# Optimization experiments

Measured on AMD Instinct MI355X. Metric: run time of the kernel, lower is better.

## Reference

```python
import jax, jax.numpy as jnp
import numpy as np

N_NODES = 50000
N_EDGES = 625000
D = 128          # hidden_dim
H = 8            # num_heads
DH = D // H      # head_dim
L = 4            # num_layers
F_IN = 64        # in_channels
G = 64           # num graphs
BETA = 1.0
EPS = 1e-5       # layernorm eps


def _seg_softmax(s, idx, n):
    # softmax of s over segments defined by idx (segments present in idx are never empty)
    m = jax.ops.segment_max(s, idx, num_segments=n)
    e = jnp.exp(s - m[idx])
    d = jax.ops.segment_sum(e, idx, num_segments=n)
    return e / d[idx]


def _ln(x, s, b):
    mu = jnp.mean(x, axis=-1, keepdims=True)
    var = jnp.var(x, axis=-1, keepdims=True)
    return (x - mu) / jnp.sqrt(var + EPS) * s + b


def _forward(x, edge_index, batch, node_W, node_b, cW1, cb1, cW2, cb2,
             qW, qb, kW, kb, vW, vb, oW, ob, bW, bb,
             f1W, f1b, f2W, f2b, n1s, n1b, n2s, n2b,
             outW1, outb1, outW2, outb2):
    N = x.shape[0]
    src, tgt = edge_index[0], edge_index[1]
    h = x @ node_W + node_b                              # [N, D]
    for l in range(L):
        # ---- dynamic curvature (attention-approximated Wasserstein) ----
        h_src, h_tgt = h[src], h[tgt]                    # [E, D]
        sim = jnp.sum(h_src * h_tgt, axis=-1) * BETA     # [E]
        alpha = _seg_softmax(sim, tgt, N)                # segment softmax over tgt
        dist = jnp.linalg.norm(h_src - h_tgt, axis=-1)   # [E]
        agg = jax.ops.segment_sum(alpha * dist, tgt, num_segments=N)
        curv = 1.0 - agg[tgt] / jnp.maximum(dist, 1e-6)  # [E]
        ce = jax.nn.relu(curv[:, None] @ cW1 + cb1) @ cW2 + cb2  # [E, D]
        # ---- CurvphormerLayer ----
        xn = _ln(h, n1s[l], n1b[l])
        q = (xn @ qW[l] + qb[l]).reshape(N, H, DH)
        k = (xn @ kW[l] + kb[l]).reshape(N, H, DH)
        v = (xn @ vW[l] + vb[l]).reshape(N, H, DH)
        scores = jnp.sum(q[src] * k[tgt], axis=-1) / (DH ** 0.5)  # [E, H]
        scores = scores + ce @ bW[l] + bb[l]                       # curvature bias
        probs = _seg_softmax(scores, tgt, N)                       # [E, H]
        msgs = (probs[..., None] * v[tgt]).reshape(-1, D)          # [E, D]
        aggm = jax.ops.segment_sum(msgs, src, num_segments=N)     # scatter to src
        h = h + (aggm @ oW[l] + ob[l])
        xn2 = _ln(h, n2s[l], n2b[l])
        h = h + (jax.nn.relu(xn2 @ f1W[l] + f1b[l]) @ f2W[l] + f2b[l])
    # ---- mean pool per graph ----
    counts = jnp.maximum(jax.ops.segment_sum(jnp.ones((N,), h.dtype), batch, num_segments=G), 1.0)
    g = jax.ops.segment_sum(h, batch, num_segments=G) / counts[:, None]
    return jax.nn.relu(g @ outW1 + outb1) @ outW2 + outb2


def setup_inputs() -> dict:
    keys = iter(jax.random.split(jax.random.key(0), 32))
    p = lambda shape, s=0.02: jax.random.normal(next(keys), shape, jnp.float32) * s
    x = jax.random.normal(next(keys), (N_NODES, F_IN), jnp.float32)
    edge_index = jax.random.randint(next(keys), (2, N_EDGES), 0, N_NODES)
    batch = jnp.sort(jax.random.randint(next(keys), (N_NODES,), 0, G))
    inp = {
        "x": x, "edge_index": edge_index, "batch": batch,
        "node_W": p((F_IN, D)), "node_b": p((D,)),
        "cW1": p((1, D)), "cb1": p((D,)), "cW2": p((D, D)), "cb2": p((D,)),
        "qW": p((L, D, D)), "qb": p((L, D)),
        "kW": p((L, D, D)), "kb": p((L, D)),
        "vW": p((L, D, D)), "vb": p((L, D)),
        "oW": p((L, D, D)), "ob": p((L, D)),
        "bW": p((L, D, H)), "bb": p((L, H)),
        "f1W": p((L, D, 4 * D)), "f1b": p((L, 4 * D)),
        "f2W": p((L, 4 * D, D)), "f2b": p((L, D)),
        "n1s": jnp.ones((L, D), jnp.float32), "n1b": jnp.zeros((L, D), jnp.float32),
        "n2s": jnp.ones((L, D), jnp.float32), "n2b": jnp.zeros((L, D), jnp.float32),
        "outW1": p((D, D // 2)), "outb1": p((D // 2,)),
        "outW2": p((D // 2, 1)), "outb2": p((1,)),
    }
    return inp


def reference(x, edge_index, batch, node_W, node_b, cW1, cb1, cW2, cb2,
              qW, qb, kW, kb, vW, vb, oW, ob, bW, bb,
              f1W, f1b, f2W, f2b, n1s, n1b, n2s, n2b,
              outW1, outb1, outW2, outb2):
    return _forward(x, edge_index, batch, node_W, node_b, cW1, cb1, cW2, cb2,
                    qW, qb, kW, kb, vW, vb, oW, ob, bW, bb,
                    f1W, f1b, f2W, f2b, n1s, n1b, n2s, n2b,
                    outW1, outb1, outW2, outb2)
```

## Files before the change

kernel.cpp:

```cpp
#include <hip/hip_runtime.h>

#define NN 50000
#define NE 625000
#define DD 128
#define HH 8
#define DHH 16
#define NL 4
#define FIN 64
#define NG 64
#define LN_EPS 1e-5f
#define NSEG 129
#define NT32 1563
#define NT64 782
#define NBS 196
#define HLP 132

typedef __bf16 bf16x8_t __attribute__((ext_vector_type(8)));
typedef unsigned short ushort8_t __attribute__((ext_vector_type(8)));
typedef float f32x4_t __attribute__((ext_vector_type(4)));
union BF8 { ushort8_t u; bf16x8_t b; };

__device__ __forceinline__ void fma4(float4& a, float s, float4 w) {
  a.x = fmaf(s, w.x, a.x); a.y = fmaf(s, w.y, a.y);
  a.z = fmaf(s, w.z, a.z); a.w = fmaf(s, w.w, a.w);
}
__device__ __forceinline__ unsigned short f2bf(float f) {
  unsigned u = __float_as_uint(f);
  unsigned r = ((u >> 16) & 1u) + 0x7FFFu;
  return (unsigned short)((u + r) >> 16);
}
__device__ __forceinline__ float bf2f(unsigned short u) {
  return __uint_as_float((unsigned)u << 16);
}

__device__ __forceinline__ void ln_tile_bf32(const float* __restrict__ h, int nb,
                                             const float* __restrict__ sc,
                                             const float* __restrict__ bi,
                                             ushort* xbf) {
  int tid = threadIdx.x;
  int r = tid >> 4, l16 = tid & 15;
  int nr = nb + r; if (nr >= NN) nr = NN - 1;
  const float* hp = h + (size_t)nr * DD + l16 * 8;
  float4 a0 = *(const float4*)hp;
  float4 a1 = *(const float4*)(hp + 4);
  float sum = a0.x + a0.y + a0.z + a0.w + a1.x + a1.y + a1.z + a1.w;
  float sq  = a0.x*a0.x + a0.y*a0.y + a0.z*a0.z + a0.w*a0.w
            + a1.x*a1.x + a1.y*a1.y + a1.z*a1.z + a1.w*a1.w;
#pragma unroll
  for (int off = 8; off >= 1; off >>= 1) {
    sum += __shfl_xor(sum, off, 64);
    sq  += __shfl_xor(sq,  off, 64);
  }
  float mu   = sum * (1.0f / DD);
  float var  = sq * (1.0f / DD) - mu * mu;
  float rstd = rsqrtf(var + LN_EPS);
  int d0 = l16 * 8;
  float4 s0 = *(const float4*)(sc + d0), s1 = *(const float4*)(sc + d0 + 4);
  float4 b0 = *(const float4*)(bi + d0), b1 = *(const float4*)(bi + d0 + 4);
  ushort8_t u;
  u[0] = f2bf((a0.x - mu) * rstd * s0.x + b0.x);
  u[1] = f2bf((a0.y - mu) * rstd * s0.y + b0.y);
  u[2] = f2bf((a0.z - mu) * rstd * s0.z + b0.z);
  u[3] = f2bf((a0.w - mu) * rstd * s0.w + b0.w);
  u[4] = f2bf((a1.x - mu) * rstd * s1.x + b1.x);
  u[5] = f2bf((a1.y - mu) * rstd * s1.y + b1.y);
  u[6] = f2bf((a1.z - mu) * rstd * s1.z + b1.z);
  u[7] = f2bf((a1.w - mu) * rstd * s1.w + b1.w);
  int off = (r * 256 + l16 * 16) ^ ((r & 7) << 4);
  *(ushort8_t*)((char*)xbf + off) = u;
}

__global__ __launch_bounds__(256) void k_node_proj(const float* __restrict__ x,
                                                   const float* __restrict__ W,
                                                   const float* __restrict__ b,
                                                   float* __restrict__ h) {
  __shared__ float Wl[FIN * DD];
  __shared__ float xt[32][FIN];
  int tid = threadIdx.x;
  int nb = blockIdx.x * 32;
  for (int i = tid * 4; i < FIN * DD; i += 1024)
    *(float4*)&Wl[i] = *(const float4*)(W + i);
  for (int i = tid * 4; i < 32 * FIN; i += 1024) {
    int row = i >> 6, cc = i & 63;
    int node = nb + row; if (node >= NN) node = NN - 1;
    *(float4*)&xt[row][cc] = *(const float4*)(x + (size_t)node * FIN + cc);
  }
  __syncthreads();
  int c4 = (tid & 31) * 4;
  int r0 = (tid >> 5) * 4;
  float4 bv = *(const float4*)(b + c4);
  float4 a0 = bv, a1 = bv, a2 = bv, a3 = bv;
  for (int k = 0; k < FIN; k++) {
    float4 wv = *(const float4*)&Wl[k * DD + c4];
    fma4(a0, xt[r0][k], wv);
    fma4(a1, xt[r0 + 1][k], wv);
    fma4(a2, xt[r0 + 2][k], wv);
    fma4(a3, xt[r0 + 3][k], wv);
  }
  int n0 = nb + r0;
  if (n0 < NN)     *(float4*)(h + (size_t)n0 * DD + c4) = a0;
  if (n0 + 1 < NN) *(float4*)(h + (size_t)(n0 + 1) * DD + c4) = a1;
  if (n0 + 2 < NN) *(float4*)(h + (size_t)(n0 + 2) * DD + c4) = a2;
  if (n0 + 3 < NN) *(float4*)(h + (size_t)(n0 + 3) * DD + c4) = a3;
}

__global__ __launch_bounds__(256) void k_edge1(const int* __restrict__ src_s, const int* __restrict__ tgt_s,
                                               const float* __restrict__ h, float* __restrict__ sim,
                                               float* __restrict__ dist) {
  int gid = blockIdx.x * 256 + threadIdx.x;
  int e = gid >> 4;
  if (e >= NE) return;
  int j = gid & 15;
  int s = src_s[e], t = tgt_s[e];
  const float4* ap = (const float4*)(h + (size_t)s * DD + j * 8);
  const float4* bp = (const float4*)(h + (size_t)t * DD + j * 8);
  float4 a0 = ap[0], a1 = ap[1];
  float4 b0 = bp[0], b1 = bp[1];
  float dot = 0.f, sq = 0.f;
  dot = fmaf(a0.x, b0.x, dot); dot = fmaf(a0.y, b0.y, dot);
  dot = fmaf(a0.z, b0.z, dot); dot = fmaf(a0.w, b0.w, dot);
  dot = fmaf(a1.x, b1.x, dot); dot = fmaf(a1.y, b1.y, dot);
  dot = fmaf(a1.z, b1.z, dot); dot = fmaf(a1.w, b1.w, dot);
  float d0 = a0.x - b0.x, d1 = a0.y - b0.y, d2 = a0.z - b0.z, d3 = a0.w - b0.w;
  float d4 = a1.x - b1.x, d5 = a1.y - b1.y, d6 = a1.z - b1.z, d7 = a1.w - b1.w;
  sq = fmaf(d0, d0, sq); sq = fmaf(d1, d1, sq); sq = fmaf(d2, d2, sq); sq = fmaf(d3, d3, sq);
  sq = fmaf(d4, d4, sq); sq = fmaf(d5, d5, sq); sq = fmaf(d6, d6, sq); sq = fmaf(d7, d7, sq);
#pragma unroll
  for (int off = 8; off >= 1; off >>= 1) {
    dot += __shfl_xor(dot, off, 64);
    sq  += __shfl_xor(sq,  off, 64);
  }
  if (j == 0) {
    sim[e]  = dot;
    dist[e] = sqrtf(sq);
  }
}

__global__ __launch_bounds__(256) void k_curva(const int* __restrict__ rowstart_t,
    const int* __restrict__ eid_t, const float* __restrict__ sim,
    const float* __restrict__ dist, float* __restrict__ aggv) {
  int node = blockIdx.x * 32 + (threadIdx.x >> 3);
  if (node >= NN) return;
  int j = threadIdx.x & 7;
  int rs = rowstart_t[node], re = rowstart_t[node + 1];
  float m = -3.4e38f;
  for (int i = rs + j; i < re; i += 8) m = fmaxf(m, sim[eid_t[i]]);
#pragma unroll
  for (int off = 1; off <= 4; off <<= 1) m = fmaxf(m, __shfl_xor(m, off, 64));
  float den = 0.f, nd = 0.f;
  for (int i = rs + j; i < re; i += 8) {
    int e = eid_t[i];
    float ev = expf(sim[e] - m);
    den += ev;
    nd = fmaf(ev, dist[e], nd);
  }
#pragma unroll
  for (int off = 1; off <= 4; off <<= 1) {
    den += __shfl_xor(den, off, 64);
    nd  += __shfl_xor(nd,  off, 64);
  }
  if (j == 0) aggv[node] = den > 0.f ? nd / den : 0.f;
}

__global__ __launch_bounds__(512) void k_ln_qkv(const float* __restrict__ h,
    const float* __restrict__ n1s_l, const float* __restrict__ n1b_l,
    const ushort* __restrict__ qkvT_l,
    const float* __restrict__ qb_l, const float* __restrict__ kb_l, const float* __restrict__ vb_l,
    ushort* __restrict__ q, ushort* __restrict__ kk, ushort* __restrict__ v) {
  __shared__ __align__(16) ushort xbf[32 * DD];
  int nb = blockIdx.x * 32;
  ln_tile_bf32(h, nb, n1s_l, n1b_l, xbf);
  __syncthreads();
  int lane = threadIdx.x & 63;
  int w = threadIdx.x >> 6;
  int g = lane >> 4, c = lane & 15;
  int xr = (c & 7) << 4;
  char* xb = (char*)xbf;
  BF8 a[2][4];
#pragma unroll
  for (int nt = 0; nt < 2; nt++)
#pragma unroll
    for (int kt = 0; kt < 4; kt++)
      a[nt][kt].u = *(ushort8_t*)(xb + (((nt * 16 + c) * 256 + kt * 64 + g * 16) ^ xr));
#pragma unroll
  for (int ti = 0; ti < 3; ti++) {
    int t = w * 3 + ti;
    int m = t >> 3;
    int colb = (t & 7) * 16;
    const float* bias = (m == 0 ? qb_l : (m == 1 ? kb_l : vb_l));
    float4 bv = *(const float4*)(bias + colb + g * 4);
    f32x4_t acc0 = {bv.x, bv.y, bv.z, bv.w};
    f32x4_t acc1 = acc0;
    const ushort* wp = qkvT_l + (size_t)(m * DD + colb + c) * DD + g * 8;
#pragma unroll
    for (int kt = 0; kt < 4; kt++) {
      BF8 b; b.u = *(const ushort8_t*)(wp + kt * 32);
      acc0 = __builtin_amdgcn_mfma_f32_16x16x32_bf16(b.b, a[0][kt].b, acc0, 0, 0, 0);
      acc1 = __builtin_amdgcn_mfma_f32_16x16x32_bf16(b.b, a[1][kt].b, acc1, 0, 0, 0);
    }
    ushort* out = (m == 0 ? q : (m == 1 ? kk : v));
    int n0 = nb + c;
    if (n0 < NN) {
      ushort4 o; o.x = f2bf(acc0[0]); o.y = f2bf(acc0[1]); o.z = f2bf(acc0[2]); o.w = f2bf(acc0[3]);
      *(ushort4*)(out + (size_t)n0 * DD + colb + g * 4) = o;
    }
    int n1 = nb + 16 + c;
    if (n1 < NN) {
      ushort4 o; o.x = f2bf(acc1[0]); o.y = f2bf(acc1[1]); o.z = f2bf(acc1[2]); o.w = f2bf(acc1[3]);
      *(ushort4*)(out + (size_t)n1 * DD + colb + g * 4) = o;
    }
  }
}

__global__ __launch_bounds__(256) void k_scores(const int* __restrict__ src_s, const int* __restrict__ tgt_s,
    const ushort* __restrict__ q, const ushort* __restrict__ k,
    const float* __restrict__ dist, const float* __restrict__ aggv,
    const float* __restrict__ bp_g,
    const float* __restrict__ slope_l, const float* __restrict__ inter_l,
    float* __restrict__ escore) {
  __shared__ float lsl[NSEG * HH], lin[NSEG * HH], bp[DD];
  __shared__ float lcurv[32];
  __shared__ int   lseg[32];
  int tid = threadIdx.x;
  for (int idx = tid; idx < NSEG * HH; idx += 256) { lsl[idx] = slope_l[idx]; lin[idx] = inter_l[idx]; }
  if (tid < DD) bp[tid] = bp_g[tid];
  __syncthreads();
  int eb = blockIdx.x * 32;
  if (tid < 32) {
    int e = eb + tid;
    if (e < NE) {
      int t = tgt_s[e];
      float curv = 1.0f - aggv[t] / fmaxf(dist[e], 1e-6f);
      int lo = 0, hi = DD;
      while (lo < hi) { int mid = (lo + hi) >> 1; if (bp[mid] < curv) lo = mid + 1; else hi = mid; }
      lcurv[tid] = curv;
      lseg[tid] = lo;
    }
  }
  __syncthreads();
  int gi = blockIdx.x * 256 + tid;
  if (gi >= NE * HH) return;
  int i = gi >> 3, hh = gi & 7;
  int s = src_s[i], t = tgt_s[i];
  int li = tid >> 3;
  float curv = lcurv[li];
  int seg = lseg[li];
  float bias = fmaf(lsl[seg * HH + hh], curv, lin[seg * HH + hh]);
  const ushort8_t* qp = (const ushort8_t*)(q + (size_t)s * DD + hh * DHH);
  const ushort8_t* kp = (const ushort8_t*)(k + (size_t)t * DD + hh * DHH);
  float dot = 0.f;
#pragma unroll
  for (int ii = 0; ii < 2; ii++) {
    ushort8_t a = qp[ii], b = kp[ii];
#pragma unroll
    for (int jj = 0; jj < 8; jj++) dot = fmaf(bf2f(a[jj]), bf2f(b[jj]), dot);
  }
  escore[gi] = dot * 0.25f + bias;
  (void)t;
}

__global__ __launch_bounds__(256) void k_softmax_t(const int* __restrict__ rowstart_t,
    const int* __restrict__ eid_t, const float* __restrict__ escore, float2* __restrict__ msd) {
  int node = blockIdx.x * 32 + (threadIdx.x >> 3);
  if (node >= NN) return;
  int hh = threadIdx.x & 7;
  int rs = rowstart_t[node], re = rowstart_t[node + 1];
  float m = -3.4e38f;
  int i = rs;
  for (; i + 4 <= re; i += 4) {
    int e0 = eid_t[i], e1 = eid_t[i + 1], e2 = eid_t[i + 2], e3 = eid_t[i + 3];
    float s0 = escore[e0 * HH + hh];
    float s1 = escore[e1 * HH + hh];
    float s2 = escore[e2 * HH + hh];
    float s3 = escore[e3 * HH + hh];
    m = fmaxf(m, s0); m = fmaxf(m, s1); m = fmaxf(m, s2); m = fmaxf(m, s3);
  }
  for (; i < re; i++) m = fmaxf(m, escore[eid_t[i] * HH + hh]);
  float sum = 0.f;
  i = rs;
  for (; i + 4 <= re; i += 4) {
    int e0 = eid_t[i], e1 = eid_t[i + 1], e2 = eid_t[i + 2], e3 = eid_t[i + 3];
    float p0 = expf(escore[e0 * HH + hh] - m);
    float p1 = expf(escore[e1 * HH + hh] - m);
    float p2 = expf(escore[e2 * HH + hh] - m);
    float p3 = expf(escore[e3 * HH + hh] - m);
    sum += p0; sum += p1; sum += p2; sum += p3;
  }
  for (; i < re; i++) sum += expf(escore[eid_t[i] * HH + hh] - m);
  float2 o; o.x = m; o.y = sum > 0.f ? 1.0f / sum : 0.f;
  msd[(size_t)node * HH + hh] = o;
}

__global__ __launch_bounds__(256) void k_agg(const int* __restrict__ tgt_s,
    const int* __restrict__ rowstart,
    const float* __restrict__ escore, const float2* __restrict__ msd,
    const ushort* __restrict__ v, ushort* __restrict__ aggmb) {
  int wave = (blockIdx.x * 256 + threadIdx.x) >> 6;
  int lane = threadIdx.x & 63;
  int rs = rowstart[wave], re = rowstart[wave + 1];
  int hh = lane >> 3;
  int d = lane * 2;
  float a0 = 0.f, a1 = 0.f;
  int i = rs;
  for (; i + 4 <= re; i += 4) {
    int t0 = tgt_s[i], t1 = tgt_s[i + 1], t2 = tgt_s[i + 2], t3 = tgt_s[i + 3];
    float e0 = escore[(i    ) * HH + hh];
    float e1 = escore[(i + 1) * HH + hh];
    float e2 = escore[(i + 2) * HH + hh];
    float e3 = escore[(i + 3) * HH + hh];
    float2 m0 = msd[(size_t)t0 * HH + hh], m1 = msd[(size_t)t1 * HH + hh];
    float2 m2 = msd[(size_t)t2 * HH + hh], m3 = msd[(size_t)t3 * HH + hh];
    ushort2 v0 = *(const ushort2*)(v + (size_t)t0 * DD + d);
    ushort2 v1 = *(const ushort2*)(v + (size_t)t1 * DD + d);
    ushort2 v2 = *(const ushort2*)(v + (size_t)t2 * DD + d);
    ushort2 v3 = *(const ushort2*)(v + (size_t)t3 * DD + d);
    float p0 = expf(e0 - m0.x) * m0.y;
    float p1 = expf(e1 - m1.x) * m1.y;
    float p2 = expf(e2 - m2.x) * m2.y;
    float p3 = expf(e3 - m3.x) * m3.y;
    a0 = fmaf(p0, bf2f(v0.x), a0); a1 = fmaf(p0, bf2f(v0.y), a1);
    a0 = fmaf(p1, bf2f(v1.x), a0); a1 = fmaf(p1, bf2f(v1.y), a1);
    a0 = fmaf(p2, bf2f(v2.x), a0); a1 = fmaf(p2, bf2f(v2.y), a1);
    a0 = fmaf(p3, bf2f(v3.x), a0); a1 = fmaf(p3, bf2f(v3.y), a1);
  }
  for (; i < re; i++) {
    int t = tgt_s[i];
    float2 md = msd[(size_t)t * HH + hh];
    float prob = expf(escore[i * HH + hh] - md.x) * md.y;
    ushort2 vv = *(const ushort2*)(v + (size_t)t * DD + d);
    a0 = fmaf(prob, bf2f(vv.x), a0);
    a1 = fmaf(prob, bf2f(vv.y), a1);
  }
  ushort2 o; o.x = f2bf(a0); o.y = f2bf(a1);
  *(ushort2*)(aggmb + (size_t)wave * DD + d) = o;
}

__global__ __launch_bounds__(512) void k_attn_ffn(const ushort* __restrict__ aggmb,
    const ushort* __restrict__ oT_l, const float* __restrict__ ob_l,
    const float* __restrict__ n2s_l, const float* __restrict__ n2b_l,
    const ushort* __restrict__ f1T_l, const float* __restrict__ f1b_l,
    const ushort* __restrict__ f2T_l, const float* __restrict__ f2b_l,
    float* __restrict__ h) {
  __shared__ float hL[64 * HLP];
  __shared__ __align__(16) char ubuf[64 * 256 * 2];
  ushort* xbf = (ushort*)ubuf;
  char* xb = ubuf;
  char* tb = ubuf;
  int nb = blockIdx.x * 64;
  int tid = threadIdx.x;
  int lane = tid & 63, w = tid >> 6;
  int g = lane >> 4, c = lane & 15;
  int colb = w * 16;
  int xr = (c & 7) << 4;
  {
    float4 obv = *(const float4*)(ob_l + colb + g * 4);
    const ushort* wp = oT_l + (size_t)(colb + c) * DD + g * 8;
    BF8 b0, b1, b2, b3;
    b0.u = *(const ushort8_t*)(wp);
    b1.u = *(const ushort8_t*)(wp + 32);
    b2.u = *(const ushort8_t*)(wp + 64);
    b3.u = *(const ushort8_t*)(wp + 96);
#pragma unroll
    for (int nt = 0; nt < 4; nt++) {
      int node = nb + nt * 16 + c;
      int na = node < NN ? node : NN - 1;
      const ushort* ap = aggmb + (size_t)na * DD + g * 8;
      BF8 a0, a1, a2, a3;
      a0.u = *(const ushort8_t*)(ap);
      a1.u = *(const ushort8_t*)(ap + 32);
      a2.u = *(const ushort8_t*)(ap + 64);
      a3.u = *(const ushort8_t*)(ap + 96);
      f32x4_t acc = {obv.x, obv.y, obv.z, obv.w};
      acc = __builtin_amdgcn_mfma_f32_16x16x32_bf16(b0.b, a0.b, acc, 0, 0, 0);
      acc = __builtin_amdgcn_mfma_f32_16x16x32_bf16(b1.b, a1.b, acc, 0, 0, 0);
      acc = __builtin_amdgcn_mfma_f32_16x16x32_bf16(b2.b, a2.b, acc, 0, 0, 0);
      acc = __builtin_amdgcn_mfma_f32_16x16x32_bf16(b3.b, a3.b, acc, 0, 0, 0);
      float4 hv = *(const float4*)(h + (size_t)na * DD + colb + g * 4);
      hv.x += acc[0]; hv.y += acc[1]; hv.z += acc[2]; hv.w += acc[3];
      *(float4*)&hL[(nt * 16 + c) * HLP + colb + g * 4] = hv;
    }
  }
  __syncthreads();
  {
    int l16 = tid & 15;
    int d0 = l16 * 8;
    float4 s0 = *(const float4*)(n2s_l + d0), s1 = *(const float4*)(n2s_l + d0 + 4);
    float4 bb0 = *(const float4*)(n2b_l + d0), bb1 = *(const float4*)(n2b_l + d0 + 4);
#pragma unroll
    for (int p = 0; p < 2; p++) {
      int r = p * 32 + (tid >> 4);
      const float* hp = &hL[r * HLP + d0];
      float4 a0 = *(const float4*)hp;
      float4 a1 = *(const float4*)(hp + 4);
      float sum = a0.x + a0.y + a0.z + a0.w + a1.x + a1.y + a1.z + a1.w;
      float sq  = a0.x*a0.x + a0.y*a0.y + a0.z*a0.z + a0.w*a0.w
                + a1.x*a1.x + a1.y*a1.y + a1.z*a1.z + a1.w*a1.w;
#pragma unroll
      for (int off = 8; off >= 1; off >>= 1) {
        sum += __shfl_xor(sum, off, 64);
        sq  += __shfl_xor(sq,  off, 64);
      }
      float mu   = sum * (1.0f / DD);
      float var  = sq * (1.0f / DD) - mu * mu;
      float rstd = rsqrtf(var + LN_EPS);
      ushort8_t u;
      u[0] = f2bf((a0.x - mu) * rstd * s0.x + bb0.x);
      u[1] = f2bf((a0.y - mu) * rstd * s0.y + bb0.y);
      u[2] = f2bf((a0.z - mu) * rstd * s0.z + bb0.z);
      u[3] = f2bf((a0.w - mu) * rstd * s0.w + bb0.w);
      u[4] = f2bf((a1.x - mu) * rstd * s1.x + bb1.x);
      u[5] = f2bf((a1.y - mu) * rstd * s1.y + bb1.y);
      u[6] = f2bf((a1.z - mu) * rstd * s1.z + bb1.z);
      u[7] = f2bf((a1.w - mu) * rstd * s1.w + bb1.w);
      int off = (r * 256 + l16 * 16) ^ ((r & 7) << 4);
      *(ushort8_t*)(xb + off) = u;
    }
  }
  __syncthreads();
  BF8 a[4][4];
#pragma unroll
  for (int nt = 0; nt < 4; nt++)
#pragma unroll
    for (int kt = 0; kt < 4; kt++)
      a[nt][kt].u = *(ushort8_t*)(xb + (((nt * 16 + c) * 256 + kt * 64 + g * 16) ^ xr));
  __syncthreads();
  float4 bv2 = *(const float4*)(f2b_l + colb + g * 4);
  f32x4_t o0 = {bv2.x, bv2.y, bv2.z, bv2.w};
  f32x4_t o1 = o0, o2 = o0, o3 = o0;
#pragma unroll
  for (int ch = 0; ch < 2; ch++) {
    if (ch) __syncthreads();
#pragma unroll
    for (int ti = 0; ti < 2; ti++) {
      int ctile = w * 2 + ti;
      int col = ch * 256 + ctile * 16;
      float4 bv = *(const float4*)(f1b_l + col + g * 4);
      f32x4_t ac0 = {bv.x, bv.y, bv.z, bv.w};
      f32x4_t ac1 = ac0, ac2 = ac0, ac3 = ac0;
      const ushort* wp = f1T_l + (size_t)(col + c) * DD + g * 8;
#pragma unroll
      for (int kt = 0; kt < 4; kt++) {
        BF8 b; b.u = *(const ushort8_t*)(wp + kt * 32);
        ac0 = __builtin_amdgcn_mfma_f32_16x16x32_bf16(b.b, a[0][kt].b, ac0, 0, 0, 0);
        ac1 = __builtin_amdgcn_mfma_f32_16x16x32_bf16(b.b, a[1][kt].b, ac1, 0, 0, 0);
        ac2 = __builtin_amdgcn_mfma_f32_16x16x32_bf16(b.b, a[2][kt].b, ac2, 0, 0, 0);
        ac3 = __builtin_amdgcn_mfma_f32_16x16x32_bf16(b.b, a[3][kt].b, ac3, 0, 0, 0);
      }
      int colL = (ctile * 16 + g * 4) * 2;
      {
        int row = c;
        ushort4 o4; o4.x = f2bf(fmaxf(ac0[0], 0.f)); o4.y = f2bf(fmaxf(ac0[1], 0.f));
        o4.z = f2bf(fmaxf(ac0[2], 0.f)); o4.w = f2bf(fmaxf(ac0[3], 0.f));
        *(ushort4*)(tb + ((row * 512 + colL) ^ ((row & 7) << 4))) = o4;
      }
      {
        int row = 16 + c;
        ushort4 o4; o4.x = f2bf(fmaxf(ac1[0], 0.f)); o4.y = f2bf(fmaxf(ac1[1], 0.f));
        o4.z = f2bf(fmaxf(ac1[2], 0.f)); o4.w = f2bf(fmaxf(ac1[3], 0.f));
        *(ushort4*)(tb + ((row * 512 + colL) ^ ((row & 7) << 4))) = o4;
      }
      {
        int row = 32 + c;
        ushort4 o4; o4.x = f2bf(fmaxf(ac2[0], 0.f)); o4.y = f2bf(fmaxf(ac2[1], 0.f));
        o4.z = f2bf(fmaxf(ac2[2], 0.f)); o4.w = f2bf(fmaxf(ac2[3], 0.f));
        *(ushort4*)(tb + ((row * 512 + colL) ^ ((row & 7) << 4))) = o4;
      }
      {
        int row = 48 + c;
        ushort4 o4; o4.x = f2bf(fmaxf(ac3[0], 0.f)); o4.y = f2bf(fmaxf(ac3[1], 0.f));
        o4.z = f2bf(fmaxf(ac3[2], 0.f)); o4.w = f2bf(fmaxf(ac3[3], 0.f));
        *(ushort4*)(tb + ((row * 512 + colL) ^ ((row & 7) << 4))) = o4;
      }
    }
    __syncthreads();
    const ushort* wp2 = f2T_l + (size_t)(colb + c) * 512 + ch * 256 + g * 8;
#pragma unroll
    for (int kt = 0; kt < 8; kt++) {
      BF8 b; b.u = *(const ushort8_t*)(wp2 + kt * 32);
      BF8 t0; t0.u = *(ushort8_t*)(tb + (((c) * 512 + kt * 64 + g * 16) ^ xr));
      BF8 t1; t1.u = *(ushort8_t*)(tb + (((16 + c) * 512 + kt * 64 + g * 16) ^ xr));
      BF8 t2; t2.u = *(ushort8_t*)(tb + (((32 + c) * 512 + kt * 64 + g * 16) ^ xr));
      BF8 t3; t3.u = *(ushort8_t*)(tb + (((48 + c) * 512 + kt * 64 + g * 16) ^ xr));
      o0 = __builtin_amdgcn_mfma_f32_16x16x32_bf16(b.b, t0.b, o0, 0, 0, 0);
      o1 = __builtin_amdgcn_mfma_f32_16x16x32_bf16(b.b, t1.b, o1, 0, 0, 0);
      o2 = __builtin_amdgcn_mfma_f32_16x16x32_bf16(b.b, t2.b, o2, 0, 0, 0);
      o3 = __builtin_amdgcn_mfma_f32_16x16x32_bf16(b.b, t3.b, o3, 0, 0, 0);
    }
  }
  {
    int node = nb + c;
    if (node < NN) {
      const float* lp = &hL[c * HLP + colb + g * 4];
      float4 hv = *(const float4*)lp;
      hv.x += o0[0]; hv.y += o0[1]; hv.z += o0[2]; hv.w += o0[3];
      *(float4*)(h + (size_t)node * DD + colb + g * 4) = hv;
    }
  }
  {
    int node = nb + 16 + c;
    if (node < NN) {
      const float* lp = &hL[(16 + c) * HLP + colb + g * 4];
      float4 hv = *(const float4*)lp;
      hv.x += o1[0]; hv.y += o1[1]; hv.z += o1[2]; hv.w += o1[3];
      *(float4*)(h + (size_t)node * DD + colb + g * 4) = hv;
    }
  }
  {
    int node = nb + 32 + c;
    if (node < NN) {
      const float* lp = &hL[(32 + c) * HLP + colb + g * 4];
      float4 hv = *(const float4*)lp;
      hv.x += o2[0]; hv.y += o2[1]; hv.z += o2[2]; hv.w += o2[3];
      *(float4*)(h + (size_t)node * DD + colb + g * 4) = hv;
    }
  }
  {
    int node = nb + 48 + c;
    if (node < NN) {
      const float* lp = &hL[(48 + c) * HLP + colb + g * 4];
      float4 hv = *(const float4*)lp;
      hv.x += o3[0]; hv.y += o3[1]; hv.z += o3[2]; hv.w += o3[3];
      *(float4*)(h + (size_t)node * DD + colb + g * 4) = hv;
    }
  }
}

template <int K, int C>
__global__ void k_wt(const float* __restrict__ W, ushort* __restrict__ WT, int nm, int dstride) {
  int idx = blockIdx.x * 256 + threadIdx.x;
  if (idx >= K * C * nm) return;
  int mi = idx / (K * C), rem = idx - mi * (K * C);
  int cc = rem / K, kk2 = rem - cc * K;
  WT[(size_t)mi * dstride + cc * K + kk2] = f2bf(W[(size_t)mi * K * C + (size_t)kk2 * C + cc]);
}

__global__ void k_hist(const int* __restrict__ idxs, int* __restrict__ cnt) {
  int e = blockIdx.x * 256 + threadIdx.x;
  if (e < NE) atomicAdd(cnt + idxs[e], 1);
}

__global__ __launch_bounds__(256) void k_scan_blk(const int* __restrict__ cnt, int* __restrict__ bsum) {
  __shared__ int red[256];
  int tid = threadIdx.x;
  int idx = blockIdx.x * 256 + tid;
  red[tid] = (idx < NN) ? cnt[idx] : 0;
  __syncthreads();
  for (int off = 128; off >= 1; off >>= 1) {
    if (tid < off) red[tid] += red[tid + off];
    __syncthreads();
  }
  if (tid == 0) bsum[blockIdx.x] = red[0];
}

__global__ __launch_bounds__(256) void k_scan_top(const int* __restrict__ bsum,
                                                  int* __restrict__ boff, int* __restrict__ rowstart) {
  __shared__ int ps[256];
  int t = threadIdx.x;
  int v = (t < NBS) ? bsum[t] : 0;
  ps[t] = v;
  __syncthreads();
  for (int off = 1; off < 256; off <<= 1) {
    int x = (t >= off) ? ps[t - off] : 0;
    __syncthreads();
    ps[t] += x;
    __syncthreads();
  }
  boff[t] = ps[t] - v;
  if (t == 255) rowstart[NN] = ps[255];
}

__global__ __launch_bounds__(256) void k_scan_fin(const int* __restrict__ cnt,
                                                  const int* __restrict__ boff, int* __restrict__ rowstart) {
  __shared__ int ps[256];
  int t = threadIdx.x;
  int idx = blockIdx.x * 256 + t;
  int v = (idx < NN) ? cnt[idx] : 0;
  ps[t] = v;
  __syncthreads();
  for (int off = 1; off < 256; off <<= 1) {
    int x = (t >= off) ? ps[t - off] : 0;
    __syncthreads();
    ps[t] += x;
    __syncthreads();
  }
  if (idx < NN) rowstart[idx] = boff[blockIdx.x] + ps[t] - v;
}

__global__ void k_fill(const int* __restrict__ src, const int* __restrict__ tgt,
                       const int* __restrict__ rowstart,
                       int* __restrict__ cur, int* __restrict__ src_s, int* __restrict__ tgt_s) {
  int e = blockIdx.x * 256 + threadIdx.x;
  if (e >= NE) return;
  int s = src[e];
  int p = atomicAdd(cur + s, 1);
  int pos = rowstart[s] + p;
  src_s[pos] = s;
  tgt_s[pos] = tgt[e];
}

__global__ void k_fill_t(const int* __restrict__ tgt_s, const int* __restrict__ rowstart_t,
                         int* __restrict__ cur_t, int* __restrict__ eid_t) {
  int i = blockIdx.x * 256 + threadIdx.x;
  if (i >= NE) return;
  int t = tgt_s[i];
  int p = atomicAdd(cur_t + t, 1);
  eid_t[rowstart_t[t] + p] = i;
}

__global__ __launch_bounds__(64) void k_mbias_par(const float* __restrict__ cW2, const float* __restrict__ cb2,
                                                  const float* __restrict__ bW, const float* __restrict__ bb,
                                                  float* __restrict__ M, float* __restrict__ base) {
  int bid = blockIdx.x;
  int l = bid >> 7, d = bid & 127;
  int lane = threadIdx.x;
  int hh = lane >> 3, j0 = lane & 7;
  const float* bWl = bW + (size_t)l * DD * HH;
  float acc = 0.f;
#pragma unroll
  for (int t = 0; t < 16; t++) {
    int k = j0 + t * 8;
    acc = fmaf(cW2[d * DD + k], bWl[k * HH + hh], acc);
  }
#pragma unroll
  for (int off = 1; off <= 4; off <<= 1) acc += __shfl_xor(acc, off, 64);
  if (j0 == 0) M[(size_t)l * DD * HH + d * HH + hh] = acc;
  if (d == 0) {
    float bacc = 0.f;
#pragma unroll
    for (int t = 0; t < 16; t++) {
      int k = j0 + t * 8;
      bacc = fmaf(cb2[k], bWl[k * HH + hh], bacc);
    }
#pragma unroll
    for (int off = 1; off <= 4; off <<= 1) bacc += __shfl_xor(bacc, off, 64);
    if (j0 == 0) base[l * HH + hh] = bacc + bb[l * HH + hh];
  }
}

__global__ __launch_bounds__(128) void k_bp(const float* __restrict__ cW1, const float* __restrict__ cb1,
                                            float* __restrict__ bpg, int* __restrict__ posg) {
  __shared__ float x[DD], bp[DD];
  int tid = threadIdx.x;
  float c1v = cW1[tid], cbv = cb1[tid];
  x[tid] = (c1v == 0.f) ? __builtin_inff() : (-cbv / c1v);
  __syncthreads();
  float xv = x[tid]; int p = 0;
  for (int j = 0; j < DD; j++) {
    float xj = x[j];
    if (xj < xv || (xj == xv && j < tid)) p++;
  }
  bp[p] = xv;
  posg[tid] = p;
  __syncthreads();
  bpg[tid] = bp[tid];
}

__global__ __launch_bounds__(64) void k_pwl_tab(const float* __restrict__ cW1, const float* __restrict__ cb1,
    const int* __restrict__ posg, const float* __restrict__ Mb, const float* __restrict__ basel,
    float* __restrict__ slopeg, float* __restrict__ interg) {
  int bid = blockIdx.x;
  int l = bid / NSEG, s = bid - l * NSEG;
  int lane = threadIdx.x;
  int hh = lane >> 3, j0 = lane & 7;
  const float* M = Mb + (size_t)l * DD * HH;
  float sl = 0.f, in = 0.f;
#pragma unroll
  for (int t = 0; t < 16; t++) {
    int d = j0 + t * 8;
    float cv = cW1[d], cbv = cb1[d];
    int p = posg[d];
    bool act = (cv == 0.f) ? (cbv > 0.f) : ((cv > 0.f) ? (p < s) : (p >= s));
    float m = act ? M[d * HH + hh] : 0.f;
    sl = fmaf(cv, m, sl);
    in = fmaf(cbv, m, in);
  }
#pragma unroll
  for (int off = 1; off <= 4; off <<= 1) {
    sl += __shfl_xor(sl, off, 64);
    in += __shfl_xor(in, off, 64);
  }
  if (j0 == 0) {
    size_t o = (size_t)l * NSEG * HH + s * HH + hh;
    slopeg[o] = sl;
    interg[o] = in + basel[l * HH + hh];
  }
}

__global__ void k_bounds(const int* __restrict__ batch, int* __restrict__ gstart, int* __restrict__ gend) {
  int n = blockIdx.x * 256 + threadIdx.x;
  if (n >= NN) return;
  int b = batch[n];
  if (n == 0 || batch[n - 1] != b) gstart[b] = n;
  if (n == NN - 1 || batch[n + 1] != b) gend[b] = n + 1;
}

__global__ __launch_bounds__(256) void k_pool_part(const float* __restrict__ h,
    const int* __restrict__ batch, float* __restrict__ gpool) {
  int tid = threadIdx.x;
  int d = tid & 127, sub = tid >> 7;
  int n0 = blockIdx.x * 256;
  int nend = n0 + 256; if (nend > NN) nend = NN;
  float run = 0.f; int gcur = -1;
  for (int n = n0 + sub; n < nend; n += 2) {
    int g = batch[n];
    if (g != gcur) {
      if (gcur >= 0) atomicAdd(gpool + (size_t)gcur * DD + d, run);
      run = 0.f; gcur = g;
    }
    run += h[(size_t)n * DD + d];
  }
  if (gcur >= 0) atomicAdd(gpool + (size_t)gcur * DD + d, run);
}

__global__ __launch_bounds__(256) void k_head(const float* __restrict__ gpool,
    const int* __restrict__ gstart, const int* __restrict__ gend,
    const float* __restrict__ W1, const float* __restrict__ b1,
    const float* __restrict__ W2, const float* __restrict__ b2, float* __restrict__ out) {
  __shared__ float mid[NG * 64];
  int tid = threadIdx.x;
  for (int idx = tid; idx < NG * 64; idx += 256) {
    int g = idx >> 6, j = idx & 63;
    int cnt = gend[g] - gstart[g]; if (cnt < 1) cnt = 1;
    float rc = 1.0f / (float)cnt;
    float acc = 0.f;
    for (int d = 0; d < DD; d++) acc = fmaf(gpool[g * DD + d], W1[d * 64 + j], acc);
    mid[idx] = fmaxf(fmaf(acc, rc, b1[j]), 0.f);
  }
  __syncthreads();
  if (tid < NG) {
    float acc = b2[0];
    for (int j = 0; j < 64; j++) acc = fmaf(mid[tid * 64 + j], W2[j], acc);
    out[tid] = acc;
  }
}

extern "C" void kernel_launch(void* const* d_in, const int* in_sizes, int n_in,
                              void* d_out, int out_size, void* d_ws, size_t ws_size,
                              hipStream_t stream) {
  const float* x      = (const float*)d_in[0];
  const int*   ei     = (const int*)d_in[1];
  const int*   batch  = (const int*)d_in[2];
  const float* node_W = (const float*)d_in[3];
  const float* node_b = (const float*)d_in[4];
  const float* cW1    = (const float*)d_in[5];
  const float* cb1    = (const float*)d_in[6];
  const float* cW2    = (const float*)d_in[7];
  const float* cb2    = (const float*)d_in[8];
  const float* qW     = (const float*)d_in[9];
  const float* qb     = (const float*)d_in[10];
  const float* kW     = (const float*)d_in[11];
  const float* kb     = (const float*)d_in[12];
  const float* vW     = (const float*)d_in[13];
  const float* vb     = (const float*)d_in[14];
  const float* oW     = (const float*)d_in[15];
  const float* ob     = (const float*)d_in[16];
  const float* bW     = (const float*)d_in[17];
  const float* bb     = (const float*)d_in[18];
  const float* f1W    = (const float*)d_in[19];
  const float* f1b    = (const float*)d_in[20];
  const float* f2W    = (const float*)d_in[21];
  const float* f2b    = (const float*)d_in[22];
  const float* n1s    = (const float*)d_in[23];
  const float* n1b    = (const float*)d_in[24];
  const float* n2s    = (const float*)d_in[25];
  const float* n2b    = (const float*)d_in[26];
  const float* outW1  = (const float*)d_in[27];
  const float* outb1  = (const float*)d_in[28];
  const float* outW2  = (const float*)d_in[29];
  const float* outb2  = (const float*)d_in[30];

  const int* src = ei;
  const int* tgt = ei + NE;

  char* wp = (char*)d_ws;
  auto alloc = [&](size_t bytes) { void* p = (void*)wp; wp += (bytes + 255) & ~(size_t)255; return p; };
  float*    h       = (float*)alloc((size_t)NN * DD * 4);
  ushort*   q       = (ushort*)alloc((size_t)NN * DD * 2);
  ushort*   kk      = (ushort*)alloc((size_t)NN * DD * 2);
  ushort*   v       = (ushort*)alloc((size_t)NN * DD * 2);
  ushort*   aggmb   = (ushort*)alloc((size_t)NN * DD * 2);
  float*    sim     = (float*)alloc((size_t)NE * 4);
  float*    dist    = (float*)alloc((size_t)NE * 4);
  float*    escore  = (float*)alloc((size_t)NE * HH * 4);
  float2*   msd     = (float2*)alloc((size_t)NN * HH * 8);
  float*    aggv    = (float*)alloc((size_t)NN * 4);
  float*    Mb      = (float*)alloc((size_t)NL * DD * HH * 4);
  float*    basel   = (float*)alloc((size_t)NL * HH * 4);
  float*    bpg     = (float*)alloc((size_t)DD * 4);
  int*      posg    = (int*)alloc((size_t)DD * 4);
  float*    slopeg  = (float*)alloc((size_t)NL * NSEG * HH * 4);
  float*    interg  = (float*)alloc((size_t)NL * NSEG * HH * 4);
  int*      rowstart= (int*)alloc((size_t)(NN + 1) * 4);
  int*      rowstart_t = (int*)alloc((size_t)(NN + 1) * 4);
  int*      eid_t   = (int*)alloc((size_t)NE * 4);
  int*      src_s   = (int*)alloc((size_t)NE * 4);
  int*      tgt_s   = (int*)alloc((size_t)NE * 4);
  int*      cnt     = (int*)alloc((size_t)NN * 4);
  int*      cur     = (int*)alloc((size_t)NN * 4);
  int*      cnt_t   = (int*)alloc((size_t)NN * 4);
  int*      cur_t   = (int*)alloc((size_t)NN * 4);
  int*      bsum    = (int*)alloc((size_t)NBS * 4);
  int*      boff    = (int*)alloc((size_t)256 * 4);
  int*      gstart  = (int*)alloc((size_t)NG * 4);
  int*      gend    = (int*)alloc((size_t)NG * 4);
  float*    gpool   = (float*)alloc((size_t)NG * DD * 4);
  ushort*   qkvT    = (ushort*)alloc((size_t)NL * 3 * DD * DD * 2);
  ushort*   oT      = (ushort*)alloc((size_t)NL * DD * DD * 2);
  ushort*   f1T     = (ushort*)alloc((size_t)NL * DD * 512 * 2);
  ushort*   f2T     = (ushort*)alloc((size_t)NL * 512 * DD * 2);
  (void)in_sizes; (void)n_in; (void)out_size; (void)ws_size;

  hipMemsetAsync(cnt, 0, NN * 4, stream);
  hipMemsetAsync(cur, 0, NN * 4, stream);
  hipMemsetAsync(cnt_t, 0, NN * 4, stream);
  hipMemsetAsync(cur_t, 0, NN * 4, stream);
  hipMemsetAsync(gstart, 0, NG * 4, stream);
  hipMemsetAsync(gend, 0, NG * 4, stream);
  hipMemsetAsync(gpool, 0, NG * DD * 4, stream);
  k_hist<<<(NE + 255) / 256, 256, 0, stream>>>(src, cnt);
  k_scan_blk<<<NBS, 256, 0, stream>>>(cnt, bsum);
  k_scan_top<<<1, 256, 0, stream>>>(bsum, boff, rowstart);
  k_scan_fin<<<NBS, 256, 0, stream>>>(cnt, boff, rowstart);
  k_fill<<<(NE + 255) / 256, 256, 0, stream>>>(src, tgt, rowstart, cur, src_s, tgt_s);
  k_hist<<<(NE + 255) / 256, 256, 0, stream>>>(tgt, cnt_t);
  k_scan_blk<<<NBS, 256, 0, stream>>>(cnt_t, bsum);
  k_scan_top<<<1, 256, 0, stream>>>(bsum, boff, rowstart_t);
  k_scan_fin<<<NBS, 256, 0, stream>>>(cnt_t, boff, rowstart_t);
  k_fill_t<<<(NE + 255) / 256, 256, 0, stream>>>(tgt_s, rowstart_t, cur_t, eid_t);
  k_mbias_par<<<NL * DD, 64, 0, stream>>>(cW2, cb2, bW, bb, Mb, basel);
  k_bp<<<1, 128, 0, stream>>>(cW1, cb1, bpg, posg);
  k_pwl_tab<<<NL * NSEG, 64, 0, stream>>>(cW1, cb1, posg, Mb, basel, slopeg, interg);
  k_bounds<<<(NN + 255) / 256, 256, 0, stream>>>(batch, gstart, gend);
  k_wt<DD, DD><<<(NL * DD * DD + 255) / 256, 256, 0, stream>>>(qW, qkvT,               NL, 3 * DD * DD);
  k_wt<DD, DD><<<(NL * DD * DD + 255) / 256, 256, 0, stream>>>(kW, qkvT + DD * DD,     NL, 3 * DD * DD);
  k_wt<DD, DD><<<(NL * DD * DD + 255) / 256, 256, 0, stream>>>(vW, qkvT + 2 * DD * DD, NL, 3 * DD * DD);
  k_wt<DD, DD><<<(NL * DD * DD + 255) / 256, 256, 0, stream>>>(oW, oT, NL, DD * DD);
  k_wt<DD, 512><<<(NL * DD * 512 + 255) / 256, 256, 0, stream>>>(f1W, f1T, NL, DD * 512);
  k_wt<512, DD><<<(NL * DD * 512 + 255) / 256, 256, 0, stream>>>(f2W, f2T, NL, DD * 512);
  k_node_proj<<<NT32, 256, 0, stream>>>(x, node_W, node_b, h);

  for (int l = 0; l < NL; l++) {
    k_edge1<<<(NE * 16 + 255) / 256, 256, 0, stream>>>(src_s, tgt_s, h, sim, dist);
    k_curva<<<NT32, 256, 0, stream>>>(rowstart_t, eid_t, sim, dist, aggv);
    k_ln_qkv<<<NT32, 512, 0, stream>>>(h, n1s + l * DD, n1b + l * DD,
        qkvT + (size_t)l * 3 * DD * DD,
        qb + l * DD, kb + l * DD, vb + l * DD, q, kk, v);
    k_scores<<<(NE * HH + 255) / 256, 256, 0, stream>>>(src_s, tgt_s, q, kk,
        dist, aggv, bpg,
        slopeg + (size_t)l * NSEG * HH, interg + (size_t)l * NSEG * HH,
        escore);
    k_softmax_t<<<NT32, 256, 0, stream>>>(rowstart_t, eid_t, escore, msd);
    k_agg<<<NN / 4, 256, 0, stream>>>(tgt_s, rowstart, escore, msd, v, aggmb);
    k_attn_ffn<<<NT64, 512, 0, stream>>>(aggmb, oT + (size_t)l * DD * DD, ob + l * DD,
        n2s + l * DD, n2b + l * DD,
        f1T + (size_t)l * DD * 512, f1b + (size_t)l * 4 * DD,
        f2T + (size_t)l * 512 * DD, f2b + l * DD, h);
  }
  k_pool_part<<<(NN + 255) / 256, 256, 0, stream>>>(h, batch, gpool);
  k_head<<<1, 256, 0, stream>>>(gpool, gstart, gend, outW1, outb1, outW2, outb2, (float*)d_out);
}
```

Baseline: 1.372 ms.

## Fuse attention score computation into target-segment softmax kernel

Merges the per-edge score kernel into the per-target softmax kernel. Each thread group now walks its node's incoming edges, computes the curvature bias and q·k dot, writes the score and tracks the max in a single pass. The target key row and aggv are loaded once per node, and the next edge's q is software-prefetched. This removes a kernel launch and a full re-read of escore for the max pass. In exchange, per-edge parallelism becomes per-node, which exposes degree imbalance, and each edge now needs an eid indirection plus a serial binary search per head.

```diff
diff --git a/kernel.cpp b/kernel.cpp
--- a/kernel.cpp
+++ b/kernel.cpp
@@ -212,81 +212,59 @@
   }
 }
 
-__global__ __launch_bounds__(256) void k_scores(const int* __restrict__ src_s, const int* __restrict__ tgt_s,
+__global__ __launch_bounds__(256) void k_scores_sm(const int* __restrict__ src_s,
+    const int* __restrict__ rowstart_t, const int* __restrict__ eid_t,
     const ushort* __restrict__ q, const ushort* __restrict__ k,
     const float* __restrict__ dist, const float* __restrict__ aggv,
     const float* __restrict__ bp_g,
     const float* __restrict__ slope_l, const float* __restrict__ inter_l,
-    float* __restrict__ escore) {
+    float* __restrict__ escore, float2* __restrict__ msd) {
   __shared__ float lsl[NSEG * HH], lin[NSEG * HH], bp[DD];
-  __shared__ float lcurv[32];
-  __shared__ int   lseg[32];
   int tid = threadIdx.x;
   for (int idx = tid; idx < NSEG * HH; idx += 256) { lsl[idx] = slope_l[idx]; lin[idx] = inter_l[idx]; }
   if (tid < DD) bp[tid] = bp_g[tid];
   __syncthreads();
-  int eb = blockIdx.x * 32;
-  if (tid < 32) {
-    int e = eb + tid;
-    if (e < NE) {
-      int t = tgt_s[e];
-      float curv = 1.0f - aggv[t] / fmaxf(dist[e], 1e-6f);
-      int lo = 0, hi = DD;
-      while (lo < hi) { int mid = (lo + hi) >> 1; if (bp[mid] < curv) lo = mid + 1; else hi = mid; }
-      lcurv[tid] = curv;
-      lseg[tid] = lo;
-    }
-  }
-  __syncthreads();
-  int gi = blockIdx.x * 256 + tid;
-  if (gi >= NE * HH) return;
-  int i = gi >> 3, hh = gi & 7;
-  int s = src_s[i], t = tgt_s[i];
-  int li = tid >> 3;
-  float curv = lcurv[li];
-  int seg = lseg[li];
-  float bias = fmaf(lsl[seg * HH + hh], curv, lin[seg * HH + hh]);
-  const ushort8_t* qp = (const ushort8_t*)(q + (size_t)s * DD + hh * DHH);
-  const ushort8_t* kp = (const ushort8_t*)(k + (size_t)t * DD + hh * DHH);
-  float dot = 0.f;
-#pragma unroll
-  for (int ii = 0; ii < 2; ii++) {
-    ushort8_t a = qp[ii], b = kp[ii];
-#pragma unroll
-    for (int jj = 0; jj < 8; jj++) dot = fmaf(bf2f(a[jj]), bf2f(b[jj]), dot);
-  }
-  escore[gi] = dot * 0.25f + bias;
-  (void)t;
-}
-
-__global__ __launch_bounds__(256) void k_softmax_t(const int* __restrict__ rowstart_t,
-    const int* __restrict__ eid_t, const float* __restrict__ escore, float2* __restrict__ msd) {
-  int node = blockIdx.x * 32 + (threadIdx.x >> 3);
+  int node = blockIdx.x * 32 + (tid >> 3);
   if (node >= NN) return;
-  int hh = threadIdx.x & 7;
+  int hh = tid & 7;
   int rs = rowstart_t[node], re = rowstart_t[node + 1];
+  float av = aggv[node];
+  const ushort8_t* kp = (const ushort8_t*)(k + (size_t)node * DD + hh * DHH);
+  ushort8_t k0 = kp[0], k1 = kp[1];
   float m = -3.4e38f;
   int i = rs;
-  for (; i + 4 <= re; i += 4) {
-    int e0 = eid_t[i], e1 = eid_t[i + 1], e2 = eid_t[i + 2], e3 = eid_t[i + 3];
-    float s0 = escore[e0 * HH + hh];
-    float s1 = escore[e1 * HH + hh];
-    float s2 = escore[e2 * HH + hh];
-    float s3 = escore[e3 * HH + hh];
-    m = fmaxf(m, s0); m = fmaxf(m, s1); m = fmaxf(m, s2); m = fmaxf(m, s3);
-  }
-  for (; i < re; i++) m = fmaxf(m, escore[eid_t[i] * HH + hh]);
+  int e_n = 0, s_n = 0; float dd_n = 0.f; ushort8_t q0_n = {}, q1_n = {};
+  if (i < re) {
+    e_n = eid_t[i]; s_n = src_s[e_n]; dd_n = dist[e_n];
+    const ushort8_t* qp = (const ushort8_t*)(q + (size_t)s_n * DD + hh * DHH);
+    q0_n = qp[0]; q1_n = qp[1];
+  }
+  while (i < re) {
+    int e = e_n; float dd = dd_n;
+    ushort8_t q0 = q0_n, q1 = q1_n;
+    int j = i + 1;
+    if (j < re) {
+      e_n = eid_t[j]; s_n = src_s[e_n]; dd_n = dist[e_n];
+      const ushort8_t* qp = (const ushort8_t*)(q + (size_t)s_n * DD + hh * DHH);
+      q0_n = qp[0]; q1_n = qp[1];
+    }
+    float curv = 1.0f - av / fmaxf(dd, 1e-6f);
+    int lo = 0, hi = DD;
+    while (lo < hi) { int mid = (lo + hi) >> 1; if (bp[mid] < curv) lo = mid + 1; else hi = mid; }
+    float bias = fmaf(lsl[lo * HH + hh], curv, lin[lo * HH + hh]);
+    float dot = 0.f;
+#pragma unroll
+    for (int jj = 0; jj < 8; jj++) dot = fmaf(bf2f(q0[jj]), bf2f(k0[jj]), dot);
+#pragma unroll
+    for (int jj = 0; jj < 8; jj++) dot = fmaf(bf2f(q1[jj]), bf2f(k1[jj]), dot);
+    float sc = dot * 0.25f + bias;
+    escore[e * HH + hh] = sc;
+    m = fmaxf(m, sc);
+    i = j;
+  }
   float sum = 0.f;
-  i = rs;
-  for (; i + 4 <= re; i += 4) {
-    int e0 = eid_t[i], e1 = eid_t[i + 1], e2 = eid_t[i + 2], e3 = eid_t[i + 3];
-    float p0 = expf(escore[e0 * HH + hh] - m);
-    float p1 = expf(escore[e1 * HH + hh] - m);
-    float p2 = expf(escore[e2 * HH + hh] - m);
-    float p3 = expf(escore[e3 * HH + hh] - m);
-    sum += p0; sum += p1; sum += p2; sum += p3;
-  }
-  for (; i < re; i++) sum += expf(escore[eid_t[i] * HH + hh] - m);
+  for (i = rs; i < re; i++)
+    sum += expf(escore[eid_t[i] * HH + hh] - m);
   float2 o; o.x = m; o.y = sum > 0.f ? 1.0f / sum : 0.f;
   msd[(size_t)node * HH + hh] = o;
 }
@@ -343,7 +321,6 @@
     float* __restrict__ h) {
   __shared__ float hL[64 * HLP];
   __shared__ __align__(16) char ubuf[64 * 256 * 2];
-  ushort* xbf = (ushort*)ubuf;
   char* xb = ubuf;
   char* tb = ubuf;
   int nb = blockIdx.x * 64;
@@ -845,11 +822,10 @@
     k_ln_qkv<<<NT32, 512, 0, stream>>>(h, n1s + l * DD, n1b + l * DD,
         qkvT + (size_t)l * 3 * DD * DD,
         qb + l * DD, kb + l * DD, vb + l * DD, q, kk, v);
-    k_scores<<<(NE * HH + 255) / 256, 256, 0, stream>>>(src_s, tgt_s, q, kk,
+    k_scores_sm<<<NT32, 256, 0, stream>>>(src_s, rowstart_t, eid_t, q, kk,
         dist, aggv, bpg,
         slopeg + (size_t)l * NSEG * HH, interg + (size_t)l * NSEG * HH,
-        escore);
-    k_softmax_t<<<NT32, 256, 0, stream>>>(rowstart_t, eid_t, escore, msd);
+        escore, msd);
     k_agg<<<NN / 4, 256, 0, stream>>>(tgt_s, rowstart, escore, msd, v, aggmb);
     k_attn_ffn<<<NT64, 512, 0, stream>>>(aggmb, oT + (size_t)l * DD * DD, ob + l * DD,
         n2s + l * DD, n2b + l * DD,
```

Result: slower. 1.407 ms (+2.6%).
